# Kernel optimization log

Measured on AMD Instinct MI355X. Metric: run time of the kernel, lower is better.

## Reference

```python
import jax, jax.numpy as jnp
import numpy as np

NEG_INF = -jnp.inf
BIG_NEG = -1.0e9


def setup_inputs() -> dict:
    key = jax.random.key(0)
    ks = jax.random.split(key, 8)
    B, S, H = 8, 2048, 1024
    x = jax.random.normal(ks[0], (B, S, H), dtype=jnp.float32)
    attention_mask = jax.random.randint(ks[1], (B, S), 0, 2).astype(jnp.bool_)
    # keep first token always valid so no row is fully padded by the pad mask
    attention_mask = attention_mask.at[:, 0].set(True)
    scale = 0.02
    Wq = jax.random.normal(ks[2], (H, H), dtype=jnp.float32) * scale
    bq = jax.random.normal(ks[3], (H,), dtype=jnp.float32) * scale
    Wk = jax.random.normal(ks[4], (H, H), dtype=jnp.float32) * scale
    bk = jax.random.normal(ks[5], (H,), dtype=jnp.float32) * scale
    Wv = jax.random.normal(ks[6], (H, H), dtype=jnp.float32) * scale
    bv = jax.random.normal(ks[7], (H,), dtype=jnp.float32) * scale
    return {"x": x, "attention_mask": attention_mask, "Wq": Wq, "bq": bq,
            "Wk": Wk, "bk": bk, "Wv": Wv, "bv": bv}


def reference(x, attention_mask, Wq, bq, Wk, bk, Wv, bv):
    H = x.shape[-1]
    scale = jnp.sqrt(jnp.float32(H))
    # torch.nn.Linear: x @ W.T + b
    Q = jnp.einsum('bsh,oh->bso', x, Wq) + bq
    K = jnp.einsum('bsh,oh->bso', x, Wk) + bk
    V = jnp.einsum('bsh,oh->bso', x, Wv) + bv
    scores = jnp.einsum('bqh,bkh->bqk', Q, K) / scale  # [B,S,S]
    # faithful to masked_fill(tril(scores)==0, -inf): masks upper triangle
    # AND any lower-triangle score that is exactly zero
    scores = jnp.where(jnp.tril(scores) == 0, NEG_INF, scores)
    pad = attention_mask[:, :, None] & attention_mask[:, None, :]  # [B,S,S]
    scores = jnp.where(pad, scores, NEG_INF)
    # replace -inf with -1e9 (fully-masked rows -> uniform softmax, as in torch)
    scores = jnp.where(jnp.isneginf(scores), BIG_NEG, scores)
    attn = jax.nn.softmax(scores, axis=-1)
    return jnp.einsum('bqk,bkh->bqh', attn, V)
```

## Files before the change

### kernel.cpp

```cpp
#include <hip/hip_runtime.h>
#include <stdint.h>

typedef __bf16 bf16x8 __attribute__((ext_vector_type(8)));
typedef float f32x4 __attribute__((ext_vector_type(4)));

#define BB 8
#define SS 2048
#define HH 1024

#define TILE_B   32768ll
#define NTRI     136
#define BATCH_B  (NTRI * TILE_B)

#define OFF_Q      0ll
#define OFF_K      33554432ll
#define OFF_VTC    67108864ll
#define OFF_MASK   100663296ll
#define OFF_MEANV  100679680ll
#define OFF_VIDX   100712448ll
#define OFF_NV     100777984ll
#define OFF_XSUM   100778048ll
#define OFF_QCTL   100843520ll
#define OFF_QUEUE  100843584ll
#define OFF_SQ     100846656ll
#define OFF_PQ     100851008ll
#define OFF_TMP    101711872ll
#define OFF_XC     (OFF_TMP)
#define OFF_WBF    (OFF_TMP + 33554432ll)
#define OFF_SCORES (OFF_TMP + 39845888ll)

__device__ __forceinline__ unsigned short f2bf(float f) {
  unsigned int u = __float_as_uint(f);
  u += 0x7FFFu + ((u >> 16) & 1u);
  return (unsigned short)(u >> 16);
}
__device__ __forceinline__ float bf2f(unsigned short u) {
  return __uint_as_float(((unsigned int)u) << 16);
}

__device__ __forceinline__ void gl_lds16(const void* g, void* l) {
  __builtin_amdgcn_global_load_lds(
      (const __attribute__((address_space(1))) void*)g,
      (__attribute__((address_space(3))) void*)l, 16, 0, 0);
}

__global__ __launch_bounds__(1024) void canon_mask(
    const unsigned char* __restrict__ m, unsigned char* __restrict__ out) {
  __shared__ int cnt[4];
  const int t = threadIdx.x;
  if (t < 4) cnt[t] = 0;
  __syncthreads();
  uint4 v = ((const uint4*)m)[t];
  const unsigned char* pb = (const unsigned char*)&v;
  int loc[4] = {0, 0, 0, 0};
#pragma unroll
  for (int j = 0; j < 16; ++j)
    if (pb[j]) loc[j & 3]++;
#pragma unroll
  for (int r = 0; r < 4; ++r)
    if (loc[r]) atomicAdd(&cnt[r], loc[r]);
  __syncthreads();
  const int c0 = cnt[0], c1 = cnt[1], c2 = cnt[2], c3 = cnt[3];
  unsigned char ob[16];
  if (c0 > 0 && c1 == 0 && c2 == 0 && c3 == 0) {
    const int* mi = (const int*)m;
#pragma unroll
    for (int j = 0; j < 16; ++j) ob[j] = mi[t * 16 + j] ? 1 : 0;
  } else if (c0 == 0 && (c2 > 0 || c3 > 0)) {
    const float* mf = (const float*)m;
#pragma unroll
    for (int j = 0; j < 16; ++j) ob[j] = (mf[t * 16 + j] != 0.0f) ? 1 : 0;
  } else {
#pragma unroll
    for (int j = 0; j < 16; ++j) ob[j] = pb[j] ? 1 : 0;
  }
  ((uint4*)out)[t] = *(const uint4*)ob;
}

__global__ __launch_bounds__(256) void build_compact(
    const unsigned char* __restrict__ mask, int* __restrict__ vidx,
    int* __restrict__ nv, int* __restrict__ qctl, int* __restrict__ queue,
    int* __restrict__ sq, int* __restrict__ pq) {
  const int b = blockIdx.x;
  const int t = threadIdx.x;
  __shared__ int cnt[256];
  __shared__ int totalS;
  const unsigned char* mb = mask + b * SS;
  unsigned char m[8];
  int c = 0;
#pragma unroll
  for (int j = 0; j < 8; ++j) { m[j] = mb[t * 8 + j]; c += m[j] ? 1 : 0; }
  cnt[t] = c;
  __syncthreads();
  int base = 0;
  for (int i = 0; i < t; ++i) base += cnt[i];
  if (t == 255) totalS = base + c;
  int pos = base;
  int* vb = vidx + b * SS;
#pragma unroll
  for (int j = 0; j < 8; ++j) {
    const int s = t * 8 + j;
    if (m[j]) { vb[pos] = s; ++pos; }
  }
  __syncthreads();
  const int total = totalS;
  if (t == 0) {
    nv[b] = total;
    const int ntile = (total + 255) >> 8;
    {
      const int n = ntile * 12;
      const int qb = atomicAdd(&qctl[1], n);
      int k = 0;
      for (int tt = 0; tt < ntile; ++tt)
        for (int z = 0; z < 3; ++z)
          for (int bn = 0; bn < 4; ++bn)
            queue[qb + (k++)] = (((b << 3) | tt) << 4) | (z << 2) | bn;
    }
    const int nt = (total + 127) >> 7;
    {
      const int ntri = nt * (nt + 1) / 2;
      const int qb = atomicAdd(&qctl[3], ntri);
      for (int t0 = 0; t0 < ntri; ++t0) sq[qb + t0] = (b << 8) | t0;
    }
    {
      const int n = nt * 8;
      const int qb = atomicAdd(&qctl[5], n);
      int k = 0;
      for (int bm = nt - 1; bm >= 0; --bm)
        for (int bn = 0; bn < 8; ++bn)
          pq[qb + (k++)] = (b << 7) | (bm << 3) | bn;
    }
  }
  for (int idx = total + t; idx < SS; idx += 256) vb[idx] = 0;
}

__global__ __launch_bounds__(256) void cvt_xc(
    const float* __restrict__ x, const int* __restrict__ vidx,
    const int* __restrict__ nv, unsigned short* __restrict__ Xc) {
  const int j = blockIdx.x;
  const int b = blockIdx.y;
  const int n = nv[b];
  const int ntile = (n + 255) >> 8;
  if (j >= ntile * 256) return;
  const int t = threadIdx.x;
  unsigned short* dst = Xc + ((long)b * SS + j) * HH + t * 4;
  if (j < n) {
    const float* src = x + ((long)b * SS + vidx[b * SS + j]) * HH + t * 4;
    float4 v = *(const float4*)src;
    ushort4 o;
    o.x = f2bf(v.x); o.y = f2bf(v.y); o.z = f2bf(v.z); o.w = f2bf(v.w);
    *(ushort4*)dst = o;
  } else {
    ushort4 z = {0, 0, 0, 0};
    *(ushort4*)dst = z;
  }
}

__global__ void cvt_w3(const float* __restrict__ Wq, const float* __restrict__ Wk,
                       const float* __restrict__ Wv, unsigned short* __restrict__ out) {
  const int z = blockIdx.y;
  const float* src = (z == 0) ? Wq : (z == 1) ? Wk : Wv;
  unsigned short* dst = out + (long)z * (HH * HH);
  const int n4 = HH * HH / 4;
  int i = blockIdx.x * 256 + threadIdx.x;
  for (; i < n4; i += 256 * 256) {
    float4 v = ((const float4*)src)[i];
    ushort4 o;
    o.x = f2bf(v.x); o.y = f2bf(v.y); o.z = f2bf(v.z); o.w = f2bf(v.w);
    ((ushort4*)dst)[i] = o;
  }
}

__global__ __launch_bounds__(256) void xsum_cols(
    const float* __restrict__ x, float* __restrict__ xsum) {
  const int b = blockIdx.y;
  const int sc = blockIdx.x;
  const int t = threadIdx.x;
  const float* base = x + ((long)b * SS + sc * 64) * HH + t * 4;
  float s0 = 0.f, s1 = 0.f, s2 = 0.f, s3 = 0.f;
#pragma unroll 4
  for (int i = 0; i < 64; ++i) {
    float4 u = *(const float4*)(base + (long)i * HH);
    s0 += u.x; s1 += u.y; s2 += u.z; s3 += u.w;
  }
  float* xs = xsum + b * HH + t * 4;
  atomicAdd(&xs[0], s0); atomicAdd(&xs[1], s1);
  atomicAdd(&xs[2], s2); atomicAdd(&xs[3], s3);
}

__global__ __launch_bounds__(256) void meanv_dot(
    const float* __restrict__ xsum, const unsigned short* __restrict__ Wvbf,
    const float* __restrict__ bv, float* __restrict__ meanV) {
  const int b = blockIdx.y;
  const int wave = threadIdx.x >> 6, lane = threadIdx.x & 63;
  const int h = blockIdx.x * 4 + wave;
  const unsigned short* wrow = Wvbf + (long)h * HH + lane * 16;
  const float* xs = xsum + b * HH + lane * 16;
  float s = 0.f;
#pragma unroll
  for (int j = 0; j < 4; ++j) {
    ushort4 u = *(const ushort4*)(wrow + j * 4);
    s += bf2f(u.x) * xs[j * 4 + 0] + bf2f(u.y) * xs[j * 4 + 1] +
         bf2f(u.z) * xs[j * 4 + 2] + bf2f(u.w) * xs[j * 4 + 3];
  }
#pragma unroll
  for (int off = 32; off > 0; off >>= 1) s += __shfl_down(s, off, 64);
  if (lane == 0) meanV[(long)b * HH + h] = s + 2048.0f * bv[h];
}

__global__ __launch_bounds__(256) void fixup_masked(
    float* __restrict__ out, const unsigned char* __restrict__ mask,
    const float* __restrict__ sums) {
  const long row = blockIdx.x;
  if (mask[row]) return;
  const long b = row >> 11;
  const int t = threadIdx.x;
  float4 v = ((const float4*)(sums + b * HH))[t];
  v.x *= (1.f / 2048.f); v.y *= (1.f / 2048.f);
  v.z *= (1.f / 2048.f); v.w *= (1.f / 2048.f);
  ((float4*)(out + row * HH))[t] = v;
}

__global__ __launch_bounds__(512, 2) void gemm256q(
    const unsigned short* __restrict__ Xc,
    const unsigned short* __restrict__ Bbase, long bStride,
    char* __restrict__ Cq, char* __restrict__ Ck, char* __restrict__ VtcOut,
    const float* __restrict__ biasq, const float* __restrict__ biask,
    const float* __restrict__ biasv,
    const int* __restrict__ queue, int* __restrict__ qctl) {
  extern __shared__ char smem[];
  int* bc = (int*)(smem + 131072);
  const int tid = threadIdx.x;
  const int wave = tid >> 6, lane = tid & 63;
  const int wr = wave >> 2, wc = wave & 3;
  const int l15 = lane & 15, l4 = lane >> 4;

  const int srow = tid >> 3;
  const int gslot = (tid & 7) ^ (srow & 7);
  const int ldsStageW = wave << 10;
  const int sw0 = ((l4 ^ (l15 & 7)) << 4);
  const int sw1 = (((4 + l4) ^ (l15 & 7)) << 4);
  const int aB0 = (wr << 14) + l15 * 128 + sw0;
  const int aB1 = (wr << 14) + l15 * 128 + sw1;
  const int bB0 = 32768 + ((wc >> 1) << 14) + (((wc & 1) << 6) + l15) * 128 + sw0;
  const int bB1 = 32768 + ((wc >> 1) << 14) + (((wc & 1) << 6) + l15) * 128 + sw1;
  const int rl0 = (wr << 7) + (l4 << 2);
  const int cl0 = (wc << 6) + l15;
  const int qcnt = qctl[1];

  for (;;) {
    __syncthreads();
    if (tid == 0) *bc = atomicAdd(&qctl[0], 1);
    __syncthreads();
    const int idx = *bc;
    if (idx >= qcnt) break;
    const int e = queue[idx];
    const int bm = e >> 4;
    const int bz = (e >> 2) & 3;
    const int bn = e & 3;
    const int b = bm >> 3;
    const int rInB = (bm & 7) * 256;

    const char* gA = (const char*)Xc + ((long)b * SS + rInB + srow) * 2048 +
                     gslot * 16;
    const char* gB = (const char*)(Bbase + (long)bz * bStride) +
                     ((long)bn * 256 + srow) * 2048 + gslot * 16;

#define STG(kt_, type_, buf_) do { \
    const char* _g = (((type_) < 2) ? gA : gB) + \
                     (((type_) & 1) ? 262144 : 0) + ((long)(kt_) << 7); \
    char* _l = smem + ((buf_) << 16) + (((type_) >> 1) << 15) + \
               (((type_) & 1) << 14) + ldsStageW; \
    gl_lds16(_g, _l); \
    gl_lds16(_g + 131072, _l + 8192); } while (0)

    f32x4 acc[8][4];
    const f32x4 z4 = {0.f, 0.f, 0.f, 0.f};
#pragma unroll
    for (int m = 0; m < 8; ++m)
#pragma unroll
      for (int n = 0; n < 4; ++n) acc[m][n] = z4;

    STG(0, 0, 0); STG(0, 1, 0); STG(0, 2, 0); STG(0, 3, 0);
    STG(1, 0, 1); STG(1, 1, 1); STG(1, 2, 1); STG(1, 3, 1);
    asm volatile("s_waitcnt vmcnt(8)" ::: "memory");
    __builtin_amdgcn_s_barrier();
    __builtin_amdgcn_sched_barrier(0);

    bf16x8 aC[4][2], bLo[2][2], bHi[2][2];

    for (int it = 0; it < 8; ++it) {
#pragma unroll
      for (int g = 0; g < 8; ++g) {
        const int buf = (g < 4) ? 0 : 65536;
        const int q = g & 3;
        if (q == 0) {
#pragma unroll
          for (int mm = 0; mm < 4; ++mm) {
            aC[mm][0] = *(const bf16x8*)(smem + buf + aB0 + mm * 2048);
            aC[mm][1] = *(const bf16x8*)(smem + buf + aB1 + mm * 2048);
          }
#pragma unroll
          for (int nn = 0; nn < 2; ++nn) {
            bLo[nn][0] = *(const bf16x8*)(smem + buf + bB0 + nn * 2048);
            bLo[nn][1] = *(const bf16x8*)(smem + buf + bB1 + nn * 2048);
          }
        } else if (q == 1) {
#pragma unroll
          for (int nn = 0; nn < 2; ++nn) {
            bHi[nn][0] = *(const bf16x8*)(smem + buf + bB0 + (2 + nn) * 2048);
            bHi[nn][1] = *(const bf16x8*)(smem + buf + bB1 + (2 + nn) * 2048);
          }
        } else if (q == 2) {
#pragma unroll
          for (int mm = 0; mm < 4; ++mm) {
            aC[mm][0] = *(const bf16x8*)(smem + buf + aB0 + (4 + mm) * 2048);
            aC[mm][1] = *(const bf16x8*)(smem + buf + aB1 + (4 + mm) * 2048);
          }
        }
        {
          const int u = it * 8 + g - 2;
          if (u >= 0) {
            const int kt = 2 + (u >> 2);
            if (kt < 16) {
              if (g == 0)      STG(kt, 0, 1);
              else if (g == 1) STG(kt, 1, 1);
              else if (g == 2) STG(kt, 2, 0);
              else if (g == 3) STG(kt, 3, 0);
              else if (g == 4) STG(kt, 0, 0);
              else if (g == 5) STG(kt, 1, 0);
              else if (g == 6) STG(kt, 2, 1);
              else             STG(kt, 3, 1);
            }
          }
        }
        __builtin_amdgcn_s_barrier();
        asm volatile("s_waitcnt lgkmcnt(0)" ::: "memory");
        __builtin_amdgcn_sched_barrier(0);
        __builtin_amdgcn_s_setprio(1);
        if (q == 0) {
#pragma unroll
          for (int mm = 0; mm < 4; ++mm)
#pragma unroll
            for (int nn = 0; nn < 2; ++nn) {
              acc[mm][nn] = __builtin_amdgcn_mfma_f32_16x16x32_bf16(
                  aC[mm][0], bLo[nn][0], acc[mm][nn], 0, 0, 0);
              acc[mm][nn] = __builtin_amdgcn_mfma_f32_16x16x32_bf16(
                  aC[mm][1], bLo[nn][1], acc[mm][nn], 0, 0, 0);
            }
        } else if (q == 1) {
#pragma unroll
          for (int mm = 0; mm < 4; ++mm)
#pragma unroll
            for (int nn = 0; nn < 2; ++nn) {
              acc[mm][2 + nn] = __builtin_amdgcn_mfma_f32_16x16x32_bf16(
                  aC[mm][0], bHi[nn][0], acc[mm][2 + nn], 0, 0, 0);
              acc[mm][2 + nn] = __builtin_amdgcn_mfma_f32_16x16x32_bf16(
                  aC[mm][1], bHi[nn][1], acc[mm][2 + nn], 0, 0, 0);
            }
        } else if (q == 2) {
#pragma unroll
          for (int mm = 0; mm < 4; ++mm)
#pragma unroll
            for (int nn = 0; nn < 2; ++nn) {
              acc[4 + mm][2 + nn] = __builtin_amdgcn_mfma_f32_16x16x32_bf16(
                  aC[mm][0], bHi[nn][0], acc[4 + mm][2 + nn], 0, 0, 0);
              acc[4 + mm][2 + nn] = __builtin_amdgcn_mfma_f32_16x16x32_bf16(
                  aC[mm][1], bHi[nn][1], acc[4 + mm][2 + nn], 0, 0, 0);
            }
        } else {
#pragma unroll
          for (int mm = 0; mm < 4; ++mm)
#pragma unroll
            for (int nn = 0; nn < 2; ++nn) {
              acc[4 + mm][nn] = __builtin_amdgcn_mfma_f32_16x16x32_bf16(
                  aC[mm][0], bLo[nn][0], acc[4 + mm][nn], 0, 0, 0);
              acc[4 + mm][nn] = __builtin_amdgcn_mfma_f32_16x16x32_bf16(
                  aC[mm][1], bLo[nn][1], acc[4 + mm][nn], 0, 0, 0);
            }
        }
        __builtin_amdgcn_s_setprio(0);
        __builtin_amdgcn_sched_barrier(0);
        if (q == 3) {
          if (g == 3 && it == 7)
            asm volatile("s_waitcnt vmcnt(0)" ::: "memory");
          else
            asm volatile("s_waitcnt vmcnt(4)" ::: "memory");
        }
        __builtin_amdgcn_s_barrier();
        asm volatile("" ::: "memory");
      }
    }
#undef STG

    if (bz < 2) {
      const float* bias = (bz == 0) ? biasq : biask;
#pragma unroll
      for (int n = 0; n < 4; ++n) {
        const int cl = cl0 + n * 16;
        const float bv = bias[bn * 256 + cl];
        const int colx = cl ^ (l4 << 4);
#pragma unroll
        for (int m = 0; m < 8; ++m) {
          const int rl = rl0 + m * 16;
#pragma unroll
          for (int r = 0; r < 4; ++r)
            *(unsigned short*)(smem + (rl + r) * 512 + colx * 2) =
                f2bf(acc[m][n][r] + bv);
        }
      }
      __syncthreads();
      unsigned short* C = (unsigned short*)((bz == 0) ? Cq : Ck);
      const long rowg0 = (long)b * SS + rInB;
      const long colb0 = (long)bn * 512;
#pragma unroll
      for (int i = 0; i < 16; ++i) {
        const int s2 = i * 512 + tid;
        const int row = s2 >> 5;
        const int cb = s2 & 31;
        const int lb = (row * 512 + (cb << 4)) ^ (((row >> 2) & 3) << 5);
        *(uint4*)((char*)C + (rowg0 + row) * 2048 + colb0 + (cb << 4)) =
            *(const uint4*)(smem + lb);
      }
    } else {
#pragma unroll
      for (int n = 0; n < 4; ++n) {
        const int h = cl0 + n * 16;
        const float bv = biasv[bn * 256 + h];
        const int xr = (h & 7) << 4;
#pragma unroll
        for (int m = 0; m < 8; ++m) {
          const int s0a = rl0 + m * 16;
          uint2 w;
          w.x = (unsigned)f2bf(acc[m][n][0] + bv) |
                ((unsigned)f2bf(acc[m][n][1] + bv) << 16);
          w.y = (unsigned)f2bf(acc[m][n][2] + bv) |
                ((unsigned)f2bf(acc[m][n][3] + bv) << 16);
          *(uint2*)(smem + h * 512 + ((s0a * 2) ^ xr)) = w;
        }
      }
      __syncthreads();
      char* VtB = VtcOut + (long)b * (SS * HH * 2) + (long)(bm & 7) * 512;
#pragma unroll
      for (int i = 0; i < 16; ++i) {
        const int s2 = i * 512 + tid;
        const int h = s2 >> 5;
        const int cb = s2 & 31;
        const int lb = h * 512 + ((cb << 4) ^ ((h & 7) << 4));
        *(uint4*)(VtB + (long)(bn * 256 + h) * 4096 + cb * 16) =
            *(const uint4*)(smem + lb);
      }
    }
  }
}

__global__ __launch_bounds__(256, 2) void gemm128s(
    const unsigned short* __restrict__ Qc, const unsigned short* __restrict__ Kc,
    char* __restrict__ scoresBase, const int* __restrict__ sq,
    int* __restrict__ qctl) {
  __shared__ __align__(16) char smem[65536];
  __shared__ int bc;
  const int tid = threadIdx.x;
  const int wave = tid >> 6, lane = tid & 63;
  const int wr = wave >> 1, wc = wave & 1;
  const int l15 = lane & 15, l4 = lane >> 4;

  const int s0 = tid, s1 = tid + 256;
  const int rA0 = ((s0 >> 3) << 1) | (((s0 >> 2) & 1) ^ ((s0 >> 4) & 1));
  const int cA0 = (s0 & 3) ^ (rA0 & 3);
  const int rA1 = ((s1 >> 3) << 1) | (((s1 >> 2) & 1) ^ ((s1 >> 4) & 1));
  const int cA1 = (s1 & 3) ^ (rA1 & 3);
  const int ldsL0 = wave << 10;
  const int ldsL1 = 4096 + (wave << 10);
  const int baseSwz = ((l15 * 64 + (l4 << 4)) ^ ((l15 & 7) << 4));
  const int rdA = (wr << 12) + baseSwz;
  const int rdB = 8192 + (wc << 12) + baseSwz;
  const int rl0 = (wr << 6) + (l4 << 2);
  const int cl0 = (wc << 6) + l15;
  const int qcnt = qctl[3];

  for (;;) {
    __syncthreads();
    if (tid == 0) bc = atomicAdd(&qctl[2], 1);
    __syncthreads();
    const int idx = bc;
    if (idx >= qcnt) break;
    const int e = sq[idx];
    const int bz = e >> 8;
    int t0 = e & 255, bm = 0, a_ = 0;
    while (a_ + bm + 1 <= t0) { ++bm; a_ += bm; }
    const int bn = t0 - a_;

    const unsigned short* A = Qc + (long)bz * SS * HH;
    const unsigned short* B = Kc + (long)bz * SS * HH;
    const char* aG0 = (const char*)A + (long)(bm * 128 + rA0) * 2048 + cA0 * 16;
    const char* aG1 = (const char*)A + (long)(bm * 128 + rA1) * 2048 + cA1 * 16;
    const char* bG0 = (const char*)B + (long)(bn * 128 + rA0) * 2048 + cA0 * 16;
    const char* bG1 = (const char*)B + (long)(bn * 128 + rA1) * 2048 + cA1 * 16;

#define STG(t_) do { \
    char* _p = smem + (((t_) & 3) << 14); \
    const long _ko = (long)(t_) << 6; \
    gl_lds16(aG0 + _ko, _p + ldsL0); \
    gl_lds16(aG1 + _ko, _p + ldsL1); \
    gl_lds16(bG0 + _ko, _p + 8192 + ldsL0); \
    gl_lds16(bG1 + _ko, _p + 8192 + ldsL1); } while (0)

    f32x4 acc[4][4];
    const f32x4 z4 = {0.f, 0.f, 0.f, 0.f};
#pragma unroll
    for (int m = 0; m < 4; ++m)
#pragma unroll
      for (int n = 0; n < 4; ++n) acc[m][n] = z4;

    STG(0); STG(1); STG(2);
    asm volatile("s_waitcnt vmcnt(8)" ::: "memory");
    __builtin_amdgcn_s_barrier();
    __builtin_amdgcn_sched_barrier(0);

    const int kT = 32;
    for (int t = 0; t < kT; ++t) {
      if (t + 3 < kT) STG(t + 3);
      const char* bufp = smem + ((t & 3) << 14);
      bf16x8 af[4], bg[4];
#pragma unroll
      for (int m = 0; m < 4; ++m)
        af[m] = *(const bf16x8*)(bufp + rdA + (m << 10));
#pragma unroll
      for (int n = 0; n < 4; ++n)
        bg[n] = *(const bf16x8*)(bufp + rdB + (n << 10));
      __builtin_amdgcn_s_setprio(1);
#pragma unroll
      for (int m = 0; m < 4; ++m)
#pragma unroll
        for (int n = 0; n < 4; ++n)
          acc[m][n] = __builtin_amdgcn_mfma_f32_16x16x32_bf16(af[m], bg[n],
                                                              acc[m][n], 0, 0, 0);
      __builtin_amdgcn_s_setprio(0);
      __builtin_amdgcn_sched_barrier(0);
      if (t + 3 < kT)       asm volatile("s_waitcnt vmcnt(8)" ::: "memory");
      else if (t + 3 == kT) asm volatile("s_waitcnt vmcnt(4)" ::: "memory");
      else if (t + 2 == kT) asm volatile("s_waitcnt vmcnt(0)" ::: "memory");
      if (t + 1 < kT) {
        __builtin_amdgcn_s_barrier();
        __builtin_amdgcn_sched_barrier(0);
        asm volatile("" ::: "memory");
      }
    }
#undef STG

    char* Ct = scoresBase + (long)bz * BATCH_B + (long)t0 * TILE_B;
    __syncthreads();
#pragma unroll
    for (int m = 0; m < 4; ++m)
#pragma unroll
      for (int r = 0; r < 4; ++r) {
        const int ql = rl0 + m * 16 + r;
        const int qg = bm * 128 + ql;
#pragma unroll
        for (int n = 0; n < 4; ++n) {
          const int kg = bn * 128 + cl0 + n * 16;
          const float v = (kg <= qg) ? acc[m][n][r] * 0.03125f : -1.0e9f;
          const int colx = (cl0 + n * 16) ^ (l4 << 4);
          *(unsigned short*)(smem + ql * 256 + colx * 2) = f2bf(v);
        }
      }
    __syncthreads();
#pragma unroll
    for (int i = 0; i < 8; ++i) {
      const int s2 = i * 256 + tid;
      const int row = s2 >> 4;
      const int cb = s2 & 15;
      const int lb = row * 256 + ((cb << 4) ^ (((row >> 2) & 3) << 5));
      *(uint4*)(Ct + (long)row * 256 + (cb << 4)) = *(const uint4*)(smem + lb);
    }
  }
}

__global__ __launch_bounds__(256) void softmax_tri(char* __restrict__ base,
                                                   const int* __restrict__ nv) {
  const int r = blockIdx.x;
  const int bz = blockIdx.y;
  if (r >= nv[bz]) return;
  const int bm = r >> 7;
  const int w = (bm + 1) << 7;
  char* bb = base + (long)bz * BATCH_B +
             (long)(bm * (bm + 1) / 2) * TILE_B + (long)(r & 127) * 256;
  const int t = threadIdx.x;
  const bool act = (t << 3) < w;
  const int bn = t >> 4;
  const int cl = (t << 3) & 127;
  char* slot = bb + (long)bn * TILE_B + (long)cl * 2;
  float v[8];
  float m = -3.0e38f;
  if (act) {
    ushort4 u0 = ((const ushort4*)slot)[0];
    ushort4 u1 = ((const ushort4*)slot)[1];
    v[0] = bf2f(u0.x); v[1] = bf2f(u0.y); v[2] = bf2f(u0.z); v[3] = bf2f(u0.w);
    v[4] = bf2f(u1.x); v[5] = bf2f(u1.y); v[6] = bf2f(u1.z); v[7] = bf2f(u1.w);
#pragma unroll
    for (int k = 0; k < 8; ++k) m = fmaxf(m, v[k]);
  }
  __shared__ float red[8];
#pragma unroll
  for (int off = 32; off > 0; off >>= 1) m = fmaxf(m, __shfl_down(m, off, 64));
  const int wid = t >> 6, lane = t & 63;
  if (lane == 0) red[wid] = m;
  __syncthreads();
  m = fmaxf(fmaxf(red[0], red[1]), fmaxf(red[2], red[3]));
  float e[8];
  float s = 0.f;
  if (act) {
#pragma unroll
    for (int k = 0; k < 8; ++k) { e[k] = __expf(v[k] - m); s += e[k]; }
  }
#pragma unroll
  for (int off = 32; off > 0; off >>= 1) s += __shfl_down(s, off, 64);
  if (lane == 0) red[4 + wid] = s;
  __syncthreads();
  s = red[4] + red[5] + red[6] + red[7];
  const float inv = 1.0f / s;
  if (act) {
    ushort4 o0, o1;
    o0.x = f2bf(e[0] * inv); o0.y = f2bf(e[1] * inv);
    o0.z = f2bf(e[2] * inv); o0.w = f2bf(e[3] * inv);
    o1.x = f2bf(e[4] * inv); o1.y = f2bf(e[5] * inv);
    o1.z = f2bf(e[6] * inv); o1.w = f2bf(e[7] * inv);
    ((ushort4*)slot)[0] = o0;
    ((ushort4*)slot)[1] = o1;
  }
}

__global__ __launch_bounds__(256, 2) void gemm_pv(
    const char* __restrict__ attn, const unsigned short* __restrict__ Vtc,
    float* __restrict__ Out, const int* __restrict__ vidx,
    const int* __restrict__ nv, const int* __restrict__ pq,
    int* __restrict__ qctl) {
  __shared__ __align__(16) char smem[65536];
  __shared__ int bc;
  const int tid = threadIdx.x;
  const int wave = tid >> 6, lane = tid & 63;
  const int wr = wave >> 1, wc = wave & 1;
  const int l15 = lane & 15, l4 = lane >> 4;

  const int s0 = tid, s1 = tid + 256;
  const int rA0 = ((s0 >> 3) << 1) | (((s0 >> 2) & 1) ^ ((s0 >> 4) & 1));
  const int cA0 = (s0 & 3) ^ (rA0 & 3);
  const int rA1 = ((s1 >> 3) << 1) | (((s1 >> 2) & 1) ^ ((s1 >> 4) & 1));
  const int cA1 = (s1 & 3) ^ (rA1 & 3);
  const int ldsL0 = wave << 10;
  const int ldsL1 = 4096 + (wave << 10);
  const int baseSwz = ((l15 * 64 + (l4 << 4)) ^ ((l15 & 7) << 4));
  const int rdA = (wr << 12) + baseSwz;
  const int rdB = 8192 + (wc << 12) + baseSwz;
  const int rl0 = (wr << 6) + (l4 << 2);
  const int cl0 = (wc << 6) + l15;
  const int qcnt = qctl[5];

  for (;;) {
    __syncthreads();
    if (tid == 0) bc = atomicAdd(&qctl[4], 1);
    __syncthreads();
    const int idx = bc;
    if (idx >= qcnt) break;
    const int e = pq[idx];
    const int bz = e >> 7;
    const int bm = (e >> 3) & 15;
    const int bn = e & 7;
    const int nvb = nv[bz];

    const char* Ab = attn + (long)bz * BATCH_B +
                     (long)(bm * (bm + 1) / 2) * TILE_B;
    const unsigned short* B = Vtc + (long)bz * SS * HH;
    const char* aB0 = Ab + (long)rA0 * 256 + cA0 * 16;
    const char* aB1 = Ab + (long)rA1 * 256 + cA1 * 16;
    const char* bG0 = (const char*)(B + (long)(bn * 128 + rA0) * SS) + cA0 * 16;
    const char* bG1 = (const char*)(B + (long)(bn * 128 + rA1) * SS) + cA1 * 16;

#define STGPV(t_) do { \
    char* _p = smem + (((t_) & 3) << 14); \
    const long _aO = (long)((t_) >> 2) * TILE_B + (long)((t_) & 3) * 64; \
    const long _bO = (long)(t_) << 6; \
    gl_lds16(aB0 + _aO, _p + ldsL0); \
    gl_lds16(aB1 + _aO, _p + ldsL1); \
    gl_lds16(bG0 + _bO, _p + 8192 + ldsL0); \
    gl_lds16(bG1 + _bO, _p + 8192 + ldsL1); } while (0)

    f32x4 acc[4][4];
    const f32x4 z4 = {0.f, 0.f, 0.f, 0.f};
#pragma unroll
    for (int m = 0; m < 4; ++m)
#pragma unroll
      for (int n = 0; n < 4; ++n) acc[m][n] = z4;

    STGPV(0); STGPV(1); STGPV(2);
    asm volatile("s_waitcnt vmcnt(8)" ::: "memory");
    __builtin_amdgcn_s_barrier();
    __builtin_amdgcn_sched_barrier(0);

    const int kT = (bm + 1) * 4;
    for (int t = 0; t < kT; ++t) {
      if (t + 3 < kT) STGPV(t + 3);
      const char* bufp = smem + ((t & 3) << 14);
      bf16x8 af[4], bg[4];
#pragma unroll
      for (int m = 0; m < 4; ++m)
        af[m] = *(const bf16x8*)(bufp + rdA + (m << 10));
#pragma unroll
      for (int n = 0; n < 4; ++n)
        bg[n] = *(const bf16x8*)(bufp + rdB + (n << 10));
      __builtin_amdgcn_s_setprio(1);
#pragma unroll
      for (int m = 0; m < 4; ++m)
#pragma unroll
        for (int n = 0; n < 4; ++n)
          acc[m][n] = __builtin_amdgcn_mfma_f32_16x16x32_bf16(af[m], bg[n],
                                                              acc[m][n], 0, 0, 0);
      __builtin_amdgcn_s_setprio(0);
      __builtin_amdgcn_sched_barrier(0);
      if (t + 3 < kT)       asm volatile("s_waitcnt vmcnt(8)" ::: "memory");
      else if (t + 3 == kT) asm volatile("s_waitcnt vmcnt(4)" ::: "memory");
      else if (t + 2 == kT) asm volatile("s_waitcnt vmcnt(0)" ::: "memory");
      if (t + 1 < kT) {
        __builtin_amdgcn_s_barrier();
        __builtin_amdgcn_sched_barrier(0);
        asm volatile("" ::: "memory");
      }
    }
#undef STGPV

    __syncthreads();
#pragma unroll
    for (int m = 0; m < 4; ++m)
#pragma unroll
      for (int r = 0; r < 4; ++r) {
        const int ql = rl0 + m * 16 + r;
#pragma unroll
        for (int n = 0; n < 4; ++n) {
          const int colx = (cl0 + n * 16) ^ (l4 << 4);
          *(float*)(smem + ql * 512 + colx * 4) = acc[m][n][r];
        }
      }
    __syncthreads();
    const int* vb = vidx + (long)bz * SS;
#pragma unroll
    for (int i = 0; i < 16; ++i) {
      const int s2 = i * 256 + tid;
      const int row = s2 >> 5;
      const int cb = s2 & 31;
      const int lb = (row * 512 + (cb << 4)) ^ (((row >> 2) & 3) << 6);
      const int crow = bm * 128 + row;
      if (crow < nvb) {
        const int orig = vb[crow];
        *(uint4*)((char*)Out + (((long)bz * SS + orig) * HH) * 4 +
                  (long)bn * 512 + (cb << 4)) = *(const uint4*)(smem + lb);
      }
    }
  }
}

extern "C" void kernel_launch(void* const* d_in, const int* in_sizes, int n_in,
                              void* d_out, int out_size, void* d_ws, size_t ws_size,
                              hipStream_t stream) {
  (void)in_sizes; (void)n_in; (void)out_size; (void)ws_size;
  const float* x = (const float*)d_in[0];
  const unsigned char* mask_raw = (const unsigned char*)d_in[1];
  const float* Wq = (const float*)d_in[2];
  const float* bq = (const float*)d_in[3];
  const float* Wk = (const float*)d_in[4];
  const float* bk = (const float*)d_in[5];
  const float* Wv = (const float*)d_in[6];
  const float* bv = (const float*)d_in[7];
  char* ws = (char*)d_ws;

  unsigned short* Xc = (unsigned short*)(ws + OFF_XC);
  unsigned short* Wbf = (unsigned short*)(ws + OFF_WBF);
  unsigned short* Qc = (unsigned short*)(ws + OFF_Q);
  unsigned short* Kc = (unsigned short*)(ws + OFF_K);
  unsigned short* Vtc = (unsigned short*)(ws + OFF_VTC);
  unsigned char* mask = (unsigned char*)(ws + OFF_MASK);
  float* meanV = (float*)(ws + OFF_MEANV);
  int* vidx = (int*)(ws + OFF_VIDX);
  int* nv = (int*)(ws + OFF_NV);
  float* xsum = (float*)(ws + OFF_XSUM);
  int* qctl = (int*)(ws + OFF_QCTL);
  int* queue = (int*)(ws + OFF_QUEUE);
  int* sq = (int*)(ws + OFF_SQ);
  int* pq = (int*)(ws + OFF_PQ);

  (void)hipFuncSetAttribute((const void*)gemm256q,
                            hipFuncAttributeMaxDynamicSharedMemorySize, 131088);

  hipMemsetAsync(qctl, 0, 32, stream);
  hipMemsetAsync(xsum, 0, (size_t)BB * HH * 4, stream);
  canon_mask<<<1, 1024, 0, stream>>>(mask_raw, mask);
  build_compact<<<BB, 256, 0, stream>>>(mask, vidx, nv, qctl, queue, sq, pq);

  cvt_xc<<<dim3(SS, BB), 256, 0, stream>>>(x, vidx, nv, Xc);
  cvt_w3<<<dim3(256, 3), 256, 0, stream>>>(Wq, Wk, Wv, Wbf);

  xsum_cols<<<dim3(32, BB), 256, 0, stream>>>(x, xsum);
  meanv_dot<<<dim3(HH / 4, BB), 256, 0, stream>>>(
      xsum, Wbf + 2 * HH * HH, bv, meanV);

  gemm256q<<<256, 512, 131088, stream>>>(
      Xc, Wbf, (long)HH * HH,
      (char*)Qc, (char*)Kc, (char*)Vtc, bq, bk, bv, queue, qctl);

  gemm128s<<<512, 256, 0, stream>>>(Qc, Kc, ws + OFF_SCORES, sq, qctl);

  softmax_tri<<<dim3(SS, BB), 256, 0, stream>>>(ws + OFF_SCORES, nv);

  gemm_pv<<<512, 256, 0, stream>>>(
      ws + OFF_SCORES, Vtc, (float*)d_out, vidx, nv, pq, qctl);

  fixup_masked<<<BB * SS, 256, 0, stream>>>((float*)d_out, mask, meanV);
}
```

Before: 236.7 us.

## Fuse x column-sum with bf16 compaction and use per-batch work queues

```diff
diff --git a/kernel.cpp b/kernel.cpp
--- a/kernel.cpp
+++ b/kernel.cpp
@@ -20,10 +20,11 @@
 #define OFF_VIDX   100712448ll
 #define OFF_NV     100777984ll
 #define OFF_XSUM   100778048ll
-#define OFF_QCTL   100843520ll
-#define OFF_QUEUE  100843584ll
-#define OFF_SQ     100846656ll
-#define OFF_PQ     100851008ll
+#define OFF_CIDX   100810816ll
+#define OFF_QCTL   100876544ll
+#define OFF_QUEUE  100876800ll
+#define OFF_SQ     100879872ll
+#define OFF_PQ     100884224ll
 #define OFF_TMP    101711872ll
 #define OFF_XC     (OFF_TMP)
 #define OFF_WBF    (OFF_TMP + 33554432ll)
@@ -79,8 +80,8 @@
 
 __global__ __launch_bounds__(256) void build_compact(
     const unsigned char* __restrict__ mask, int* __restrict__ vidx,
-    int* __restrict__ nv, int* __restrict__ qctl, int* __restrict__ queue,
-    int* __restrict__ sq, int* __restrict__ pq) {
+    int* __restrict__ cidx, int* __restrict__ nv, int* __restrict__ qctl,
+    int* __restrict__ queue, int* __restrict__ sq, int* __restrict__ pq) {
   const int b = blockIdx.x;
   const int t = threadIdx.x;
   __shared__ int cnt[256];
@@ -97,10 +98,12 @@
   if (t == 255) totalS = base + c;
   int pos = base;
   int* vb = vidx + b * SS;
+  int* cb = cidx + b * SS;
 #pragma unroll
   for (int j = 0; j < 8; ++j) {
     const int s = t * 8 + j;
-    if (m[j]) { vb[pos] = s; ++pos; }
+    if (m[j]) { vb[pos] = s; cb[s] = pos; ++pos; }
+    else cb[s] = -1;
   }
   __syncthreads();
   const int total = totalS;
@@ -108,52 +111,62 @@
     nv[b] = total;
     const int ntile = (total + 255) >> 8;
     {
-      const int n = ntile * 12;
-      const int qb = atomicAdd(&qctl[1], n);
       int k = 0;
-      for (int tt = 0; tt < ntile; ++tt)
-        for (int z = 0; z < 3; ++z)
-          for (int bn = 0; bn < 4; ++bn)
-            queue[qb + (k++)] = (((b << 3) | tt) << 4) | (z << 2) | bn;
+      for (int z = 0; z < 3; ++z)
+        for (int bn = 0; bn < 4; ++bn)
+          for (int tt = 0; tt < ntile; ++tt)
+            queue[b * 96 + (k++)] = (((b << 3) | tt) << 4) | (z << 2) | bn;
+      qctl[24 + b] = k;
     }
     const int nt = (total + 127) >> 7;
     {
       const int ntri = nt * (nt + 1) / 2;
-      const int qb = atomicAdd(&qctl[3], ntri);
-      for (int t0 = 0; t0 < ntri; ++t0) sq[qb + t0] = (b << 8) | t0;
+      for (int t0 = 0; t0 < ntri; ++t0) sq[b * 136 + t0] = (b << 8) | t0;
+      qctl[32 + b] = ntri;
     }
     {
-      const int n = nt * 8;
-      const int qb = atomicAdd(&qctl[5], n);
       int k = 0;
       for (int bm = nt - 1; bm >= 0; --bm)
         for (int bn = 0; bn < 8; ++bn)
-          pq[qb + (k++)] = (b << 7) | (bm << 3) | bn;
+          pq[b * 128 + (k++)] = (b << 7) | (bm << 3) | bn;
+      qctl[40 + b] = k;
     }
   }
   for (int idx = total + t; idx < SS; idx += 256) vb[idx] = 0;
 }
 
-__global__ __launch_bounds__(256) void cvt_xc(
-    const float* __restrict__ x, const int* __restrict__ vidx,
+__global__ __launch_bounds__(256) void prep_x(
+    const float* __restrict__ x, const int* __restrict__ cidx,
+    float* __restrict__ xsum, unsigned short* __restrict__ Xc) {
+  const int b = blockIdx.y;
+  const int sc = blockIdx.x;
+  const int t = threadIdx.x;
+  float s0 = 0.f, s1 = 0.f, s2 = 0.f, s3 = 0.f;
+  for (int i = 0; i < 64; ++i) {
+    const int srow = sc * 64 + i;
+    float4 v = *(const float4*)(x + ((long)b * SS + srow) * HH + t * 4);
+    s0 += v.x; s1 += v.y; s2 += v.z; s3 += v.w;
+    const int cc = cidx[b * SS + srow];
+    if (cc >= 0) {
+      ushort4 o;
+      o.x = f2bf(v.x); o.y = f2bf(v.y); o.z = f2bf(v.z); o.w = f2bf(v.w);
+      *(ushort4*)(Xc + ((long)b * SS + cc) * HH + t * 4) = o;
+    }
+  }
+  float* xs = xsum + b * HH + t * 4;
+  atomicAdd(&xs[0], s0); atomicAdd(&xs[1], s1);
+  atomicAdd(&xs[2], s2); atomicAdd(&xs[3], s3);
+}
+
+__global__ __launch_bounds__(256) void zero_pad(
     const int* __restrict__ nv, unsigned short* __restrict__ Xc) {
-  const int j = blockIdx.x;
   const int b = blockIdx.y;
   const int n = nv[b];
   const int ntile = (n + 255) >> 8;
+  const int j = n + blockIdx.x;
   if (j >= ntile * 256) return;
-  const int t = threadIdx.x;
-  unsigned short* dst = Xc + ((long)b * SS + j) * HH + t * 4;
-  if (j < n) {
-    const float* src = x + ((long)b * SS + vidx[b * SS + j]) * HH + t * 4;
-    float4 v = *(const float4*)src;
-    ushort4 o;
-    o.x = f2bf(v.x); o.y = f2bf(v.y); o.z = f2bf(v.z); o.w = f2bf(v.w);
-    *(ushort4*)dst = o;
-  } else {
-    ushort4 z = {0, 0, 0, 0};
-    *(ushort4*)dst = z;
-  }
+  ushort4 z = {0, 0, 0, 0};
+  *(ushort4*)(Xc + ((long)b * SS + j) * HH + threadIdx.x * 4) = z;
 }
 
 __global__ void cvt_w3(const float* __restrict__ Wq, const float* __restrict__ Wk,
@@ -169,23 +182,6 @@
     o.x = f2bf(v.x); o.y = f2bf(v.y); o.z = f2bf(v.z); o.w = f2bf(v.w);
     ((ushort4*)dst)[i] = o;
   }
-}
-
-__global__ __launch_bounds__(256) void xsum_cols(
-    const float* __restrict__ x, float* __restrict__ xsum) {
-  const int b = blockIdx.y;
-  const int sc = blockIdx.x;
-  const int t = threadIdx.x;
-  const float* base = x + ((long)b * SS + sc * 64) * HH + t * 4;
-  float s0 = 0.f, s1 = 0.f, s2 = 0.f, s3 = 0.f;
-#pragma unroll 4
-  for (int i = 0; i < 64; ++i) {
-    float4 u = *(const float4*)(base + (long)i * HH);
-    s0 += u.x; s1 += u.y; s2 += u.z; s3 += u.w;
-  }
-  float* xs = xsum + b * HH + t * 4;
-  atomicAdd(&xs[0], s0); atomicAdd(&xs[1], s1);
-  atomicAdd(&xs[2], s2); atomicAdd(&xs[3], s3);
 }
 
 __global__ __launch_bounds__(256) void meanv_dot(
@@ -234,6 +230,7 @@
   const int wave = tid >> 6, lane = tid & 63;
   const int wr = wave >> 2, wc = wave & 3;
   const int l15 = lane & 15, l4 = lane >> 4;
+  const int myq = blockIdx.x & 7;
 
   const int srow = tid >> 3;
   const int gslot = (tid & 7) ^ (srow & 7);
@@ -246,15 +243,21 @@
   const int bB1 = 32768 + ((wc >> 1) << 14) + (((wc & 1) << 6) + l15) * 128 + sw1;
   const int rl0 = (wr << 7) + (l4 << 2);
   const int cl0 = (wc << 6) + l15;
-  const int qcnt = qctl[1];
 
   for (;;) {
     __syncthreads();
-    if (tid == 0) *bc = atomicAdd(&qctl[0], 1);
-    __syncthreads();
-    const int idx = *bc;
-    if (idx >= qcnt) break;
-    const int e = queue[idx];
+    if (tid == 0) {
+      int e = -1;
+      for (int qi = 0; qi < 8; ++qi) {
+        const int q = (myq + qi) & 7;
+        const int idx = atomicAdd(&qctl[q], 1);
+        if (idx < qctl[24 + q]) { e = queue[q * 96 + idx]; break; }
+      }
+      *bc = e;
+    }
+    __syncthreads();
+    const int e = *bc;
+    if (e < 0) break;
     const int bm = e >> 4;
     const int bz = (e >> 2) & 3;
     const int bn = e & 3;
@@ -464,6 +467,7 @@
   const int wave = tid >> 6, lane = tid & 63;
   const int wr = wave >> 1, wc = wave & 1;
   const int l15 = lane & 15, l4 = lane >> 4;
+  const int myq = blockIdx.x & 7;
 
   const int s0 = tid, s1 = tid + 256;
   const int rA0 = ((s0 >> 3) << 1) | (((s0 >> 2) & 1) ^ ((s0 >> 4) & 1));
@@ -477,15 +481,21 @@
   const int rdB = 8192 + (wc << 12) + baseSwz;
   const int rl0 = (wr << 6) + (l4 << 2);
   const int cl0 = (wc << 6) + l15;
-  const int qcnt = qctl[3];
 
   for (;;) {
     __syncthreads();
-    if (tid == 0) bc = atomicAdd(&qctl[2], 1);
-    __syncthreads();
-    const int idx = bc;
-    if (idx >= qcnt) break;
-    const int e = sq[idx];
+    if (tid == 0) {
+      int e = -1;
+      for (int qi = 0; qi < 8; ++qi) {
+        const int q = (myq + qi) & 7;
+        const int idx = atomicAdd(&qctl[8 + q], 1);
+        if (idx < qctl[32 + q]) { e = sq[q * 136 + idx]; break; }
+      }
+      bc = e;
+    }
+    __syncthreads();
+    const int e = bc;
+    if (e < 0) break;
     const int bz = e >> 8;
     int t0 = e & 255, bm = 0, a_ = 0;
     while (a_ + bm + 1 <= t0) { ++bm; a_ += bm; }
@@ -642,6 +652,7 @@
   const int wave = tid >> 6, lane = tid & 63;
   const int wr = wave >> 1, wc = wave & 1;
   const int l15 = lane & 15, l4 = lane >> 4;
+  const int myq = blockIdx.x & 7;
 
   const int s0 = tid, s1 = tid + 256;
   const int rA0 = ((s0 >> 3) << 1) | (((s0 >> 2) & 1) ^ ((s0 >> 4) & 1));
@@ -655,15 +666,21 @@
   const int rdB = 8192 + (wc << 12) + baseSwz;
   const int rl0 = (wr << 6) + (l4 << 2);
   const int cl0 = (wc << 6) + l15;
-  const int qcnt = qctl[5];
 
   for (;;) {
     __syncthreads();
-    if (tid == 0) bc = atomicAdd(&qctl[4], 1);
-    __syncthreads();
-    const int idx = bc;
-    if (idx >= qcnt) break;
-    const int e = pq[idx];
+    if (tid == 0) {
+      int e = -1;
+      for (int qi = 0; qi < 8; ++qi) {
+        const int q = (myq + qi) & 7;
+        const int idx = atomicAdd(&qctl[16 + q], 1);
+        if (idx < qctl[40 + q]) { e = pq[q * 128 + idx]; break; }
+      }
+      bc = e;
+    }
+    __syncthreads();
+    const int e = bc;
+    if (e < 0) break;
     const int bz = e >> 7;
     const int bm = (e >> 3) & 15;
     const int bn = e & 7;
@@ -781,6 +798,7 @@
   unsigned char* mask = (unsigned char*)(ws + OFF_MASK);
   float* meanV = (float*)(ws + OFF_MEANV);
   int* vidx = (int*)(ws + OFF_VIDX);
+  int* cidx = (int*)(ws + OFF_CIDX);
   int* nv = (int*)(ws + OFF_NV);
   float* xsum = (float*)(ws + OFF_XSUM);
   int* qctl = (int*)(ws + OFF_QCTL);
@@ -791,15 +809,16 @@
   (void)hipFuncSetAttribute((const void*)gemm256q,
                             hipFuncAttributeMaxDynamicSharedMemorySize, 131088);
 
-  hipMemsetAsync(qctl, 0, 32, stream);
+  hipMemsetAsync(qctl, 0, 256, stream);
   hipMemsetAsync(xsum, 0, (size_t)BB * HH * 4, stream);
   canon_mask<<<1, 1024, 0, stream>>>(mask_raw, mask);
-  build_compact<<<BB, 256, 0, stream>>>(mask, vidx, nv, qctl, queue, sq, pq);
-
-  cvt_xc<<<dim3(SS, BB), 256, 0, stream>>>(x, vidx, nv, Xc);
+  build_compact<<<BB, 256, 0, stream>>>(mask, vidx, cidx, nv, qctl,
+                                        queue, sq, pq);
+
+  prep_x<<<dim3(32, BB), 256, 0, stream>>>(x, cidx, xsum, Xc);
+  zero_pad<<<dim3(256, BB), 256, 0, stream>>>(nv, Xc);
   cvt_w3<<<dim3(256, 3), 256, 0, stream>>>(Wq, Wk, Wv, Wbf);
 
-  xsum_cols<<<dim3(32, BB), 256, 0, stream>>>(x, xsum);
   meanv_dot<<<dim3(HH / 4, BB), 256, 0, stream>>>(
       xsum, Wbf + 2 * HH * HH, bv, meanV);
 
```

After: 375.2 us. +58.5%, slower.
